# Optimization experiments

Measured on AMD Instinct MI355X. Metric: run time of the kernel, lower is better.

Reference implementation:

```python
import jax, jax.numpy as jnp
from jax import lax
import numpy as np

# Straight-through-estimator sign (standard BNN binarization):
# fwd: sign(x) with sign(0)=+1; bwd: pass gradient where |x|<=1 (hardtanh STE).
@jax.custom_vjp
def sign_ste(x):
    return jnp.where(x >= 0, 1.0, -1.0).astype(x.dtype)

def _sign_fwd(x):
    return sign_ste(x), x

def _sign_bwd(x, g):
    return (g * (jnp.abs(x) <= 1.0).astype(g.dtype),)

sign_ste.defvjp(_sign_fwd, _sign_bwd)

EPS = 1e-5  # BatchNorm eps (torch default)

def bn4(x, g, b):  # BatchNorm2d, training-mode batch stats, x: [N,C,H,W]
    m = x.mean((0, 2, 3), keepdims=True)
    v = x.var((0, 2, 3), keepdims=True)
    return g[None, :, None, None] * (x - m) * lax.rsqrt(v + EPS) + b[None, :, None, None]

def bn1(x, g, b):  # BatchNorm1d, x: [N,C]
    m = x.mean(0, keepdims=True)
    v = x.var(0, keepdims=True)
    return g * (x - m) * lax.rsqrt(v + EPS) + b

def bconv(x, W, b, first):
    # BinarizedConv2d: binarize weights always; binarize input except first layer.
    xb = x if first else sign_ste(x)
    y = lax.conv_general_dilated(xb, sign_ste(W), (1, 1), [(1, 1), (1, 1)],
                                 dimension_numbers=('NCHW', 'OIHW', 'NCHW'))
    return y + b[None, :, None, None]

def maxpool2(x):
    return lax.reduce_window(x, -jnp.inf, lax.max, (1, 1, 2, 2), (1, 1, 2, 2), 'VALID')

def ht(x):  # Hardtanh
    return jnp.clip(x, -1.0, 1.0)

CONV_CH = [(3, 64), (64, 128), (128, 256), (256, 256), (256, 512), (512, 512), (512, 512), (512, 512)]
LIN_CH = [(512, 512), (512, 512), (512, 10)]
POOL_AFTER = (0, 1, 3, 5, 7)  # conv indices followed by MaxPool2d

def setup_inputs():
    key = jax.random.key(0)
    ks = iter(jax.random.split(key, 64))
    d = {"x": jax.random.normal(next(ks), (256, 3, 32, 32), jnp.float32)}
    for i, (ci, co) in enumerate(CONV_CH):
        d[f"cw{i}"] = jax.random.normal(next(ks), (co, ci, 3, 3), jnp.float32) * 0.1
        d[f"cb{i}"] = jnp.zeros((co,), jnp.float32)
        d[f"cg{i}"] = jnp.ones((co,), jnp.float32)
        d[f"ct{i}"] = jnp.zeros((co,), jnp.float32)
    for i, (ci, co) in enumerate(LIN_CH):
        d[f"lw{i}"] = jax.random.normal(next(ks), (co, ci), jnp.float32) * 0.1
        d[f"lb{i}"] = jnp.zeros((co,), jnp.float32)
        d[f"lg{i}"] = jnp.ones((co,), jnp.float32)
        d[f"lt{i}"] = jnp.zeros((co,), jnp.float32)
    return d

def _forward(x, cw, cb, cg, ct, lw, lb, lg, lt):
    h = x
    for i in range(8):
        h = bconv(h, cw[i], cb[i], i == 0)
        if i in POOL_AFTER:
            h = maxpool2(h)
        h = ht(bn4(h, cg[i], ct[i]))
    h = h.reshape(h.shape[0], -1)  # [N, 512] after 5 pools on 32x32
    for i in range(3):
        h = sign_ste(h) @ sign_ste(lw[i]).T + lb[i]  # BinarizedLinear
        h = bn1(h, lg[i], lt[i])
        if i < 2:
            h = ht(h)  # Dropout is identity in eval mode
    return jax.nn.log_softmax(h, axis=-1)

def reference(x,
              cw0, cb0, cg0, ct0, cw1, cb1, cg1, ct1, cw2, cb2, cg2, ct2,
              cw3, cb3, cg3, ct3, cw4, cb4, cg4, ct4, cw5, cb5, cg5, ct5,
              cw6, cb6, cg6, ct6, cw7, cb7, cg7, ct7,
              lw0, lb0, lg0, lt0, lw1, lb1, lg1, lt1, lw2, lb2, lg2, lt2):
    cw = [cw0, cw1, cw2, cw3, cw4, cw5, cw6, cw7]
    cb = [cb0, cb1, cb2, cb3, cb4, cb5, cb6, cb7]
    cg = [cg0, cg1, cg2, cg3, cg4, cg5, cg6, cg7]
    ct = [ct0, ct1, ct2, ct3, ct4, ct5, ct6, ct7]
    lw = [lw0, lw1, lw2]
    lb = [lb0, lb1, lb2]
    lg = [lg0, lg1, lg2]
    lt = [lt0, lt1, lt2]
    return _forward(x, cw, cb, cg, ct, lw, lb, lg, lt)
```

## Files before the change

### kernel.cpp

```cpp
#include <hip/hip_runtime.h>
#include <hip/hip_bf16.h>

typedef unsigned long long u64;

#define EPSV 1e-5

__device__ __forceinline__ int imax(int a, int b) { return a > b ? a : b; }
__device__ __forceinline__ int iclamp(int v, int lo, int hi) { return v < lo ? lo : (v > hi ? hi : v); }

struct PrepArgs {
    const float* src[10];
    u64* dst[10];
    int CW[10];
    int Co[10];
    int taps[10];
    int rowbase[11];
    u64* accs;
    int naccs;
};

__global__ __launch_bounds__(256) void prep_kernel(PrepArgs a) {
    __shared__ float buf[4608];
    const int blk = blockIdx.x;
    int z = blk * 18 + threadIdx.x;
    if (threadIdx.x < 18 && z < a.naccs) a.accs[z] = 0ULL;

    int l = 0;
    while (l < 9 && blk >= a.rowbase[l + 1]) ++l;
    const int row = blk - a.rowbase[l];
    const int CW = a.CW[l];
    const int taps = a.taps[l];
    const int nf = CW * 64 * taps;
    const float* srow = a.src[l] + (size_t)row * nf;
    for (int i = threadIdx.x; i < nf; i += 256) buf[i] = srow[i];
    __syncthreads();
    const int t = threadIdx.x;
    if (t < taps * CW) {
        u64 bits = 0;
        if (taps == 9) {
            int k = t % 9, w = t / 9;
            for (int j = 0; j < 64; ++j) bits |= (u64)(buf[(w * 64 + j) * 9 + k] >= 0.f) << j;
            a.dst[l][(size_t)(k * CW + w) * a.Co[l] + row] = bits;
        } else {
            for (int j = 0; j < 64; ++j) bits |= (u64)(buf[t * 64 + j] >= 0.f) << j;
            a.dst[l][(size_t)row * CW + t] = bits;
        }
    }
}

__global__ __launch_bounds__(256) void conv0_lane(const float* __restrict__ x,
                                                  const float* __restrict__ wgt,
                                                  float* __restrict__ out,
                                                  double* __restrict__ dacc) {
    const int lane = threadIdx.x & 63;
    const int wave = threadIdx.x >> 6;
    float ws[27];
#pragma unroll
    for (int j = 0; j < 27; ++j) ws[j] = (wgt[lane * 27 + j] >= 0.f) ? 1.f : -1.f;

    const int gp0 = blockIdx.x * 32;
    const int n = gp0 >> 8;
    const int ypA = (gp0 >> 4) & 15;
    const int yb = 2 * ypA - 1;

    __shared__ float simg[3][6][34];
    const float* xb = x + (size_t)n * 3072;
    for (int t = threadIdx.x; t < 612; t += 256) {
        int ci = t / 204;
        int rem = t % 204;
        int r = rem / 34;
        int cc = rem % 34;
        int yy = yb + r;
        int xx = cc - 1;
        float v = 0.f;
        if ((unsigned)yy < 32u && (unsigned)xx < 32u) v = xb[(ci * 32 + yy) * 32 + xx];
        simg[ci][r][cc] = v;
    }
    __syncthreads();

    double s1 = 0.0, s2 = 0.0;
#pragma unroll 2
    for (int pi = 0; pi < 8; ++pi) {
        const int lp = wave * 8 + pi;
        const int gp = gp0 + lp;
        const int xp = lp & 15;
        const int rbase = 2 * (lp >> 4);
        const int cbase = 2 * xp;
        float win[3][4][4];
#pragma unroll
        for (int ci = 0; ci < 3; ++ci)
#pragma unroll
            for (int r = 0; r < 4; ++r)
#pragma unroll
                for (int c = 0; c < 4; ++c) win[ci][r][c] = simg[ci][rbase + r][cbase + c];
        float a00 = 0.f, a01 = 0.f, a10 = 0.f, a11 = 0.f;
#pragma unroll
        for (int ci = 0; ci < 3; ++ci)
#pragma unroll
            for (int ky = 0; ky < 3; ++ky)
#pragma unroll
                for (int kx = 0; kx < 3; ++kx) {
                    float wv = ws[ci * 9 + ky * 3 + kx];
                    a00 += win[ci][ky][kx] * wv;
                    a01 += win[ci][ky][kx + 1] * wv;
                    a10 += win[ci][ky + 1][kx] * wv;
                    a11 += win[ci][ky + 1][kx + 1] * wv;
                }
        float val = fmaxf(fmaxf(a00, a01), fmaxf(a10, a11));
        out[(size_t)gp * 64 + lane] = val;
        s1 += (double)val;
        s2 += (double)val * (double)val;
    }
    __shared__ double sh1[4][64], sh2[4][64];
    sh1[wave][lane] = s1;
    sh2[wave][lane] = s2;
    __syncthreads();
    if (threadIdx.x < 64) {
        double t1 = 0.0, t2 = 0.0;
#pragma unroll
        for (int r = 0; r < 4; ++r) { t1 += sh1[r][threadIdx.x]; t2 += sh2[r][threadIdx.x]; }
        double* sh = dacc + (size_t)(blockIdx.x & 7) * 1024;
        atomicAdd(&sh[2 * threadIdx.x], t1);
        atomicAdd(&sh[2 * threadIdx.x + 1], t2);
    }
}

__global__ __launch_bounds__(256) void bnpack_f(const float* __restrict__ in,
                                                const double* __restrict__ dacc,
                                                const float* __restrict__ g,
                                                const float* __restrict__ b,
                                                u64* __restrict__ act, int count) {
    __shared__ float2 sthr[64];
    if (threadIdx.x < 64) {
        int i = threadIdx.x;
        double S1 = 0.0, S2 = 0.0;
#pragma unroll
        for (int s = 0; s < 8; ++s) {
            S1 += dacc[s * 1024 + 2 * i];
            S2 += dacc[s * 1024 + 2 * i + 1];
        }
        double m = S1 / count;
        double var = S2 / count - m * m;
        double sc = (double)g[i] / sqrt(var + EPSV);
        float2 r;
        if (sc == 0.0) r = make_float2(b[i] >= 0.f ? -3.0e38f : 3.0e38f, 1.f);
        else {
            double t = m - (double)b[i] / sc;
            r = make_float2((float)t, sc > 0.0 ? 1.f : -1.f);
        }
        sthr[i] = r;
    }
    __syncthreads();
    int tid = blockIdx.x * 256 + threadIdx.x;
    int part = tid & 3;
    int word = tid >> 2;
    const float4* r4 = (const float4*)(in + (size_t)word * 64 + part * 16);
    u64 bits = 0;
#pragma unroll
    for (int q = 0; q < 4; ++q) {
        float4 v = r4[q];
        float vv[4] = {v.x, v.y, v.z, v.w};
#pragma unroll
        for (int u = 0; u < 4; ++u) {
            int c = part * 16 + q * 4 + u;
            float2 t = sthr[c];
            bool bit = (t.y > 0.f) ? (vv[u] >= t.x) : (vv[u] <= t.x);
            bits |= (u64)bit << c;
        }
    }
    bits |= __shfl_xor(bits, 1);
    bits |= __shfl_xor(bits, 2);
    if (part == 0) act[word] = bits;
}

__global__ __launch_bounds__(256) void bnpack_i(const short* __restrict__ in,
                                                const u64* __restrict__ iacc,
                                                const float* __restrict__ g,
                                                const float* __restrict__ b,
                                                u64* __restrict__ act, int Co, int wshift,
                                                int count) {
    __shared__ int2 sthr[520];
    for (int i = threadIdx.x; i < Co; i += 256) {
        long long S1 = 0, S2 = 0;
#pragma unroll
        for (int s = 0; s < 8; ++s) {
            S1 += (long long)iacc[s * 1024 + 2 * i];
            S2 += (long long)iacc[s * 1024 + 2 * i + 1];
        }
        double m = (double)S1 / count;
        double var = (double)S2 / count - m * m;
        double sc = (double)g[i] / sqrt(var + EPSV);
        int2 r;
        if (sc == 0.0) r = make_int2(b[i] >= 0.f ? (int)0x80000000 : 0x7fffffff, 0);
        else {
            double t = m - (double)b[i] / sc;
            if (t > 1.0e9) t = 1.0e9;
            if (t < -1.0e9) t = -1.0e9;
            r = (sc > 0.0) ? make_int2((int)ceil(t), 0) : make_int2((int)floor(t), 1);
        }
        sthr[(i >> 6) * 65 + (i & 63)] = r;
    }
    __syncthreads();
    int tid = blockIdx.x * 256 + threadIdx.x;
    int part = tid & 3;
    int word = tid >> 2;
    int w = word & ((1 << wshift) - 1);
    int pix = word >> wshift;
    const int4* r4 = (const int4*)(in + (size_t)pix * Co + (w << 6) + part * 16);
    u64 bits = 0;
#pragma unroll
    for (int q = 0; q < 2; ++q) {
        int4 v = r4[q];
        int words4[4] = {v.x, v.y, v.z, v.w};
#pragma unroll
        for (int u = 0; u < 4; ++u) {
#pragma unroll
            for (int h = 0; h < 2; ++h) {
                int c = part * 16 + q * 8 + u * 2 + h;
                int val = (int)(short)((h == 0) ? (words4[u] & 0xffff) : ((unsigned)words4[u] >> 16));
                int2 t = sthr[w * 65 + c];
                bool bit = t.y ? (val <= t.x) : (val >= t.x);
                bits |= (u64)bit << c;
            }
        }
    }
    bits |= __shfl_xor(bits, 1);
    bits |= __shfl_xor(bits, 2);
    if (part == 0) act[word] = bits;
}

template <int CW, int HIN, bool POOL, int WC, bool INTERIOR>
__device__ __forceinline__ void row_accum(const u64* __restrict__ inb,
                                          const u64* __restrict__ wpkT, int Co, int co,
                                          const int* yoff, const bool* ry, int* acc) {
    constexpr int HP = POOL ? HIN / 2 : HIN;
    constexpr int WS = POOL ? 4 : 3;
    constexpr int NA = POOL ? 4 : 1;
#pragma unroll 1
    for (int w0 = 0; w0 < CW; w0 += WC) {
        u64 wg[9 * WC];
#pragma unroll
        for (int k = 0; k < 9; ++k)
#pragma unroll
            for (int w = 0; w < WC; ++w)
                wg[k * WC + w] = wpkT[(size_t)(k * CW + w0 + w) * Co + co];
        u64 cur[WS][WS][WC];
#pragma unroll
        for (int d = 0; d < WS; ++d) {
            int cc = d - 1;
            int ccc = cc < 0 ? 0 : cc;
#pragma unroll
            for (int r = 0; r < WS; ++r) {
                const u64* p = inb + yoff[r] + ccc * CW + w0;
                if (WC == 1) {
                    cur[r][d][0] = p[0];
                } else {
                    ulonglong2 v = *(const ulonglong2*)p;
                    cur[r][d][0] = v.x;
                    cur[r][d][1] = v.y;
                }
            }
        }
#pragma unroll
        for (int xp = 0; xp < HP; ++xp) {
            if constexpr (POOL) {
#pragma unroll
                for (int py = 0; py < 2; ++py)
#pragma unroll
                    for (int qx = 0; qx < 2; ++qx)
#pragma unroll
                        for (int ky = 0; ky < 3; ++ky)
#pragma unroll
                            for (int kx = 0; kx < 3; ++kx) {
                                int d = qx + kx;
                                int cc = 2 * xp + d - 1;
                                if (cc >= 0 && cc < HIN) {
#pragma unroll
                                    for (int w = 0; w < WC; ++w) {
                                        int pcv = 64 - 2 * (int)__popcll(cur[py + ky][d][w] ^
                                                                         wg[(ky * 3 + kx) * WC + w]);
                                        if constexpr (INTERIOR)
                                            acc[xp * NA + py * 2 + qx] += pcv;
                                        else
                                            acc[xp * NA + py * 2 + qx] += ry[py + ky] ? pcv : 0;
                                    }
                                }
                            }
            } else {
#pragma unroll
                for (int ky = 0; ky < 3; ++ky)
#pragma unroll
                    for (int kx = 0; kx < 3; ++kx) {
                        int cc = xp + kx - 1;
                        if (cc >= 0 && cc < HIN) {
#pragma unroll
                            for (int w = 0; w < WC; ++w) {
                                int pcv = 64 - 2 * (int)__popcll(cur[ky][kx][w] ^
                                                                 wg[(ky * 3 + kx) * WC + w]);
                                if constexpr (INTERIOR)
                                    acc[xp] += pcv;
                                else
                                    acc[xp] += ry[ky] ? pcv : 0;
                            }
                        }
                    }
            }
            if (xp < HP - 1) {
                if constexpr (POOL) {
#pragma unroll
                    for (int r = 0; r < WS; ++r)
#pragma unroll
                        for (int w = 0; w < WC; ++w) {
                            cur[r][0][w] = cur[r][2][w];
                            cur[r][1][w] = cur[r][3][w];
                        }
#pragma unroll
                    for (int dd = 2; dd < 4; ++dd) {
                        int cc = 2 * (xp + 1) + dd - 1;
                        int ccc = cc >= HIN ? HIN - 1 : cc;
#pragma unroll
                        for (int r = 0; r < WS; ++r) {
                            const u64* p = inb + yoff[r] + ccc * CW + w0;
                            if (WC == 1) {
                                cur[r][dd][0] = p[0];
                            } else {
                                ulonglong2 v = *(const ulonglong2*)p;
                                cur[r][dd][0] = v.x;
                                cur[r][dd][1] = v.y;
                            }
                        }
                    }
                } else {
#pragma unroll
                    for (int r = 0; r < WS; ++r)
#pragma unroll
                        for (int w = 0; w < WC; ++w) {
                            cur[r][0][w] = cur[r][1][w];
                            cur[r][1][w] = cur[r][2][w];
                        }
                    int cc = xp + 2;
                    int ccc = cc >= HIN ? HIN - 1 : cc;
#pragma unroll
                    for (int r = 0; r < WS; ++r) {
                        const u64* p = inb + yoff[r] + ccc * CW + w0;
                        if (WC == 1) {
                            cur[r][2][0] = p[0];
                        } else {
                            ulonglong2 v = *(const ulonglong2*)p;
                            cur[r][2][0] = v.x;
                            cur[r][2][1] = v.y;
                        }
                    }
                }
            }
        }
    }
}

template <int CW, int HIN, bool POOL, int WC>
__global__ __launch_bounds__(256) void bconv_row(const u64* __restrict__ in,
                                                 const u64* __restrict__ wpkT,
                                                 short* __restrict__ out,
                                                 u64* __restrict__ iacc, int Co) {
    constexpr int HP = POOL ? HIN / 2 : HIN;
    constexpr int WS = POOL ? 4 : 3;
    constexpr int NA = POOL ? 4 : 1;
    const int lane = threadIdx.x & 63;
    const int co = blockIdx.y * 64 + lane;
    const int grow = blockIdx.x * 4 + (threadIdx.x >> 6);
    const int n = grow / HP;
    const int yp = grow % HP;
    const int y0 = (POOL ? 2 * yp : yp) - 1;
    const u64* inb = in + (size_t)n * (HIN * HIN * CW);
    int yoff[WS];
    bool ry[WS];
#pragma unroll
    for (int r = 0; r < WS; ++r) {
        int y = y0 + r;
        ry[r] = (unsigned)y < (unsigned)HIN;
        int yc = iclamp(y, 0, HIN - 1);
        yoff[r] = yc * HIN * CW;
    }
    int acc[HP * NA];
#pragma unroll
    for (int i = 0; i < HP * NA; ++i) acc[i] = 0;

    if (yp > 0 && yp < HP - 1)
        row_accum<CW, HIN, POOL, WC, true>(inb, wpkT, Co, co, yoff, ry, acc);
    else
        row_accum<CW, HIN, POOL, WC, false>(inb, wpkT, Co, co, yoff, ry, acc);

    int s1 = 0;
    long long s2 = 0;
    short* orow = out + (size_t)grow * HP * Co + co;
#pragma unroll
    for (int xp = 0; xp < HP; ++xp) {
        int ival;
        if constexpr (POOL)
            ival = imax(imax(acc[xp * 4], acc[xp * 4 + 1]), imax(acc[xp * 4 + 2], acc[xp * 4 + 3]));
        else
            ival = acc[xp];
        orow[(size_t)xp * Co] = (short)ival;
        s1 += ival;
        s2 += (long long)ival * ival;
    }

    __shared__ u64 sacc[128];
    if (threadIdx.x < 128) sacc[threadIdx.x] = 0ULL;
    __syncthreads();
    atomicAdd(&sacc[lane], (u64)(long long)s1);
    atomicAdd(&sacc[64 + lane], (u64)s2);
    __syncthreads();
    u64* sh = iacc + (size_t)(blockIdx.x & 7) * 1024;
    if (threadIdx.x < 64)
        atomicAdd(&sh[2 * (blockIdx.y * 64 + threadIdx.x)], sacc[threadIdx.x]);
    else if (threadIdx.x < 128)
        atomicAdd(&sh[2 * (blockIdx.y * 64 + threadIdx.x - 64) + 1], sacc[threadIdx.x]);
}

template <int CW, int HIN, bool POOL>
__global__ __launch_bounds__(256) void bconv_tiny(const u64* __restrict__ in,
                                                  const u64* __restrict__ wpkT,
                                                  short* __restrict__ out,
                                                  u64* __restrict__ iacc, int Co) {
    constexpr int NPX = HIN * HIN;
    constexpr int HP = POOL ? HIN / 2 : HIN;
    const int lane = threadIdx.x & 63;
    const int co = blockIdx.y * 64 + lane;
    const int n = blockIdx.x * 4 + (threadIdx.x >> 6);
    const u64* inb = in + (size_t)n * CW * NPX;
    int acc[NPX];
#pragma unroll
    for (int i = 0; i < NPX; ++i) acc[i] = 0;

#pragma unroll 2
    for (int w = 0; w < CW; ++w) {
        u64 win[NPX];
#pragma unroll
        for (int i = 0; i < NPX; ++i) win[i] = inb[i * CW + w];
#pragma unroll
        for (int k = 0; k < 9; ++k) {
            u64 wb = wpkT[(size_t)(k * CW + w) * Co + co];
            const int ky = k / 3, kx = k % 3;
#pragma unroll
            for (int py = 0; py < HIN; ++py)
#pragma unroll
                for (int px = 0; px < HIN; ++px) {
                    const int yy = py + ky - 1, xx = px + kx - 1;
                    if (yy >= 0 && yy < HIN && xx >= 0 && xx < HIN)
                        acc[py * HIN + px] += 64 - 2 * (int)__popcll(win[yy * HIN + xx] ^ wb);
                }
        }
    }

    short vals[HP * HP];
    if constexpr (POOL) {
#pragma unroll
        for (int py = 0; py < HP; ++py)
#pragma unroll
            for (int px = 0; px < HP; ++px)
                vals[py * HP + px] = (short)imax(
                    imax(acc[(2 * py) * HIN + 2 * px], acc[(2 * py) * HIN + 2 * px + 1]),
                    imax(acc[(2 * py + 1) * HIN + 2 * px], acc[(2 * py + 1) * HIN + 2 * px + 1]));
    } else {
#pragma unroll
        for (int i = 0; i < NPX; ++i) vals[i] = (short)acc[i];
    }
#pragma unroll
    for (int p = 0; p < HP * HP; ++p) out[(size_t)(n * HP * HP + p) * Co + co] = vals[p];

    long long s1 = 0, s2 = 0;
#pragma unroll
    for (int p = 0; p < HP * HP; ++p) {
        s1 += vals[p];
        s2 += (long long)vals[p] * vals[p];
    }
    __shared__ u64 sacc[128];
    if (threadIdx.x < 128) sacc[threadIdx.x] = 0ULL;
    __syncthreads();
    atomicAdd(&sacc[lane], (u64)s1);
    atomicAdd(&sacc[64 + lane], (u64)s2);
    __syncthreads();
    u64* sh = iacc + (size_t)(blockIdx.x & 7) * 1024;
    if (threadIdx.x < 64)
        atomicAdd(&sh[2 * (blockIdx.y * 64 + threadIdx.x)], sacc[threadIdx.x]);
    else if (threadIdx.x < 128)
        atomicAdd(&sh[2 * (blockIdx.y * 64 + threadIdx.x - 64) + 1], sacc[threadIdx.x]);
}

__global__ __launch_bounds__(256) void lin_kernel(const u64* __restrict__ hp,
                                                  const u64* __restrict__ wp,
                                                  const float* __restrict__ lb,
                                                  const float* __restrict__ g,
                                                  const float* __restrict__ bta,
                                                  float* __restrict__ z, int O, int applyHt) {
    int o = blockIdx.x;
    int n = threadIdx.x;
    const u64* hr = hp + n * 8;
    const u64* wr = wp + o * 8;
    int s = 0;
#pragma unroll
    for (int w = 0; w < 8; ++w) s += (int)__popcll(hr[w] ^ wr[w]);
    float val = (float)(512 - 2 * s) + lb[o];
    __shared__ double sh1[256], sh2[256];
    sh1[n] = (double)val;
    sh2[n] = (double)val * (double)val;
    __syncthreads();
    for (int st = 128; st > 0; st >>= 1) {
        if (n < st) {
            sh1[n] += sh1[n + st];
            sh2[n] += sh2[n + st];
        }
        __syncthreads();
    }
    __shared__ float sm, siv;
    if (n == 0) {
        double m = sh1[0] / 256.0;
        double var = sh2[0] / 256.0 - m * m;
        sm = (float)m;
        siv = (float)(1.0 / sqrt(var + EPSV));
    }
    __syncthreads();
    float zz = g[o] * (val - sm) * siv + bta[o];
    if (applyHt) zz = fminf(1.f, fmaxf(-1.f, zz));
    z[(size_t)n * O + o] = zz;
}

__global__ void pack_rows(const float* __restrict__ z, u64* __restrict__ hp) {
    int tid = blockIdx.x * 256 + threadIdx.x;
    int part = tid & 3;
    int word = tid >> 2;
    int ww = word & 7;
    int n = word >> 3;
    const float4* r4 = (const float4*)(z + (size_t)n * 512 + (ww << 6) + part * 16);
    u64 bits = 0;
#pragma unroll
    for (int q = 0; q < 4; ++q) {
        float4 v = r4[q];
        float vv[4] = {v.x, v.y, v.z, v.w};
#pragma unroll
        for (int u = 0; u < 4; ++u) bits |= (u64)(vv[u] >= 0.f) << (part * 16 + q * 4 + u);
    }
    bits |= __shfl_xor(bits, 1);
    bits |= __shfl_xor(bits, 2);
    if (part == 0) hp[word] = bits;
}

__global__ void lsm_kernel(const float* __restrict__ z, float* __restrict__ out) {
    int n = blockIdx.x * 64 + threadIdx.x;
    if (n >= 256) return;
    float v[10];
    float m = -1e30f;
#pragma unroll
    for (int i = 0; i < 10; ++i) {
        v[i] = z[n * 10 + i];
        m = fmaxf(m, v[i]);
    }
    float s = 0.f;
#pragma unroll
    for (int i = 0; i < 10; ++i) s += expf(v[i] - m);
    float ls = logf(s);
#pragma unroll
    for (int i = 0; i < 10; ++i) out[n * 10 + i] = v[i] - m - ls;
}

extern "C" void kernel_launch(void* const* d_in, const int* in_sizes, int n_in, void* d_out,
                              int out_size, void* d_ws, size_t ws_size, hipStream_t stream) {
    (void)in_sizes; (void)n_in; (void)out_size; (void)ws_size;
    const float* x = (const float*)d_in[0];
    const float *cw[8], *cb[8], *cg[8], *ct[8];
    for (int i = 0; i < 8; ++i) {
        cw[i] = (const float*)d_in[1 + 4 * i];
        cb[i] = (const float*)d_in[2 + 4 * i];
        cg[i] = (const float*)d_in[3 + 4 * i];
        ct[i] = (const float*)d_in[4 + 4 * i];
    }
    const float *lw[3], *lb[3], *lg[3], *lt[3];
    for (int i = 0; i < 3; ++i) {
        lw[i] = (const float*)d_in[33 + 4 * i];
        lb[i] = (const float*)d_in[34 + 4 * i];
        lg[i] = (const float*)d_in[35 + 4 * i];
        lt[i] = (const float*)d_in[36 + 4 * i];
    }

    static const int CIs[8] = {3, 64, 128, 256, 256, 512, 512, 512};
    static const int COs[8] = {64, 128, 256, 256, 512, 512, 512, 512};
    static const int HPs[8] = {16, 8, 8, 4, 4, 2, 2, 1};

    char* ws = (char*)d_ws;
    size_t off = 0;
    auto alloc = [&](size_t bytes) -> void* {
        void* p = ws + off;
        off += (bytes + 255) & ~(size_t)255;
        return p;
    };

    u64* wpkT[8] = {};
    for (int i = 1; i < 8; ++i) wpkT[i] = (u64*)alloc((size_t)COs[i] * 9 * (CIs[i] / 64) * 8);
    u64* wpl[3];
    int LO[3] = {512, 512, 10};
    for (int i = 0; i < 3; ++i) wpl[i] = (u64*)alloc((size_t)LO[i] * 8 * 8);
    u64* act[8];
    for (int i = 0; i < 8; ++i) act[i] = (u64*)alloc((size_t)256 * (COs[i] / 64) * HPs[i] * HPs[i] * 8);
    u64* fcs0 = (u64*)alloc(2048 * 8);
    u64* fcs1 = (u64*)alloc(2048 * 8);
    float* out0 = (float*)alloc((size_t)65536 * 64 * 4);
    short* i16A = (short*)alloc((size_t)16384 * 256 * 2);
    short* i16B = (short*)alloc((size_t)16384 * 256 * 2);
    float* z0 = (float*)alloc((size_t)256 * 512 * 4);
    float* z1 = (float*)alloc((size_t)256 * 512 * 4);
    float* z2 = (float*)alloc((size_t)256 * 10 * 4);
    u64* accs = (u64*)alloc((size_t)8 * 8 * 1024 * 8);
    double* dacc0 = (double*)accs;
    auto iacc = [&](int layer) { return accs + (size_t)layer * 8192; };

    PrepArgs pa;
    int rb = 0;
    for (int i = 1; i < 8; ++i) {
        int e = i - 1;
        pa.src[e] = cw[i];
        pa.dst[e] = wpkT[i];
        pa.CW[e] = CIs[i] / 64;
        pa.Co[e] = COs[i];
        pa.taps[e] = 9;
        pa.rowbase[e] = rb;
        rb += COs[i];
    }
    for (int i = 0; i < 3; ++i) {
        int e = 7 + i;
        pa.src[e] = lw[i];
        pa.dst[e] = wpl[i];
        pa.CW[e] = 8;
        pa.Co[e] = LO[i];
        pa.taps[e] = 1;
        pa.rowbase[e] = rb;
        rb += LO[i];
    }
    pa.rowbase[10] = rb;
    pa.accs = accs;
    pa.naccs = 8 * 8 * 1024;
    prep_kernel<<<rb, 256, 0, stream>>>(pa);

    conv0_lane<<<2048, 256, 0, stream>>>(x, cw[0], out0, dacc0);
    bnpack_f<<<1024, 256, 0, stream>>>(out0, dacc0, cg[0], ct[0], act[0], 65536);

    bconv_row<1, 16, true, 1><<<dim3(512, 2), 256, 0, stream>>>(act[0], wpkT[1], i16A, iacc(1), 128);
    bnpack_i<<<512, 256, 0, stream>>>(i16A, iacc(1), cg[1], ct[1], act[1], 128, 1, 16384);

    bconv_row<2, 8, false, 2><<<dim3(512, 4), 256, 0, stream>>>(act[1], wpkT[2], i16B, iacc(2), 256);
    bnpack_i<<<1024, 256, 0, stream>>>(i16B, iacc(2), cg[2], ct[2], act[2], 256, 2, 16384);

    bconv_row<4, 8, true, 2><<<dim3(256, 4), 256, 0, stream>>>(act[2], wpkT[3], i16A, iacc(3), 256);
    bnpack_i<<<256, 256, 0, stream>>>(i16A, iacc(3), cg[3], ct[3], act[3], 256, 2, 4096);

    bconv_row<4, 4, false, 2><<<dim3(256, 8), 256, 0, stream>>>(act[3], wpkT[4], i16B, iacc(4), 512);
    bnpack_i<<<512, 256, 0, stream>>>(i16B, iacc(4), cg[4], ct[4], act[4], 512, 3, 4096);

    bconv_tiny<8, 4, true><<<dim3(64, 8), 256, 0, stream>>>(act[4], wpkT[5], i16A, iacc(5), 512);
    bnpack_i<<<128, 256, 0, stream>>>(i16A, iacc(5), cg[5], ct[5], act[5], 512, 3, 1024);

    bconv_tiny<8, 2, false><<<dim3(64, 8), 256, 0, stream>>>(act[5], wpkT[6], i16B, iacc(6), 512);
    bnpack_i<<<128, 256, 0, stream>>>(i16B, iacc(6), cg[6], ct[6], act[6], 512, 3, 1024);

    bconv_tiny<8, 2, true><<<dim3(64, 8), 256, 0, stream>>>(act[6], wpkT[7], i16A, iacc(7), 512);
    bnpack_i<<<32, 256, 0, stream>>>(i16A, iacc(7), cg[7], ct[7], act[7], 512, 3, 256);

    lin_kernel<<<512, 256, 0, stream>>>(act[7], wpl[0], lb[0], lg[0], lt[0], z0, 512, 1);
    pack_rows<<<32, 256, 0, stream>>>(z0, fcs0);
    lin_kernel<<<512, 256, 0, stream>>>(fcs0, wpl[1], lb[1], lg[1], lt[1], z1, 512, 1);
    pack_rows<<<32, 256, 0, stream>>>(z1, fcs1);
    lin_kernel<<<10, 256, 0, stream>>>(fcs1, wpl[2], lb[2], lg[2], lt[2], z2, 10, 0);
    lsm_kernel<<<4, 64, 0, stream>>>(z2, (float*)d_out);
}
```

Baseline: 385.8 us.

## Vectorize loads in prep, conv0 and tiny conv; use shuffle reduction in linear

Several unrelated micro-optimizations are applied. The prep kernel copies weights with float4 loads, conv0 reads its shared-memory window with float2 loads, and bconv_tiny processes two packed input words per iteration using 128-bit loads. The linear kernel replaces its shared-memory tree reduction with wavefront shuffles plus a small cross-wave sum. These cut instruction and sync overhead in small kernels; the bconv_tiny change assumes CW is even and 16-byte alignment, and raises register pressure.

```diff
diff --git a/kernel.cpp b/kernel.cpp
--- a/kernel.cpp
+++ b/kernel.cpp
@@ -31,8 +31,9 @@
     const int CW = a.CW[l];
     const int taps = a.taps[l];
     const int nf = CW * 64 * taps;
-    const float* srow = a.src[l] + (size_t)row * nf;
-    for (int i = threadIdx.x; i < nf; i += 256) buf[i] = srow[i];
+    const float4* srow4 = (const float4*)(a.src[l] + (size_t)row * nf);
+    float4* buf4 = (float4*)buf;
+    for (int i = threadIdx.x; i < (nf >> 2); i += 256) buf4[i] = srow4[i];
     __syncthreads();
     const int t = threadIdx.x;
     if (t < taps * CW) {
@@ -82,7 +83,7 @@
 #pragma unroll 2
     for (int pi = 0; pi < 8; ++pi) {
         const int lp = wave * 8 + pi;
-        const int gp = gp0 + lp;
+        const int gp = gp0 + pi + wave * 8;
         const int xp = lp & 15;
         const int rbase = 2 * (lp >> 4);
         const int cbase = 2 * xp;
@@ -90,9 +91,14 @@
 #pragma unroll
         for (int ci = 0; ci < 3; ++ci)
 #pragma unroll
-            for (int r = 0; r < 4; ++r)
-#pragma unroll
-                for (int c = 0; c < 4; ++c) win[ci][r][c] = simg[ci][rbase + r][cbase + c];
+            for (int r = 0; r < 4; ++r) {
+                float2 t0 = *(const float2*)&simg[ci][rbase + r][cbase];
+                float2 t1 = *(const float2*)&simg[ci][rbase + r][cbase + 2];
+                win[ci][r][0] = t0.x;
+                win[ci][r][1] = t0.y;
+                win[ci][r][2] = t1.x;
+                win[ci][r][3] = t1.y;
+            }
         float a00 = 0.f, a01 = 0.f, a10 = 0.f, a11 = 0.f;
 #pragma unroll
         for (int ci = 0; ci < 3; ++ci)
@@ -433,22 +439,29 @@
 #pragma unroll
     for (int i = 0; i < NPX; ++i) acc[i] = 0;
 
-#pragma unroll 2
-    for (int w = 0; w < CW; ++w) {
-        u64 win[NPX];
-#pragma unroll
-        for (int i = 0; i < NPX; ++i) win[i] = inb[i * CW + w];
+#pragma unroll 1
+    for (int w = 0; w < CW; w += 2) {
+        u64 win[NPX][2];
+#pragma unroll
+        for (int i = 0; i < NPX; ++i) {
+            ulonglong2 v = *(const ulonglong2*)&inb[i * CW + w];
+            win[i][0] = v.x;
+            win[i][1] = v.y;
+        }
 #pragma unroll
         for (int k = 0; k < 9; ++k) {
-            u64 wb = wpkT[(size_t)(k * CW + w) * Co + co];
+            u64 wb0 = wpkT[(size_t)(k * CW + w) * Co + co];
+            u64 wb1 = wpkT[(size_t)(k * CW + w + 1) * Co + co];
             const int ky = k / 3, kx = k % 3;
 #pragma unroll
             for (int py = 0; py < HIN; ++py)
 #pragma unroll
                 for (int px = 0; px < HIN; ++px) {
                     const int yy = py + ky - 1, xx = px + kx - 1;
-                    if (yy >= 0 && yy < HIN && xx >= 0 && xx < HIN)
-                        acc[py * HIN + px] += 64 - 2 * (int)__popcll(win[yy * HIN + xx] ^ wb);
+                    if (yy >= 0 && yy < HIN && xx >= 0 && xx < HIN) {
+                        acc[py * HIN + px] += 64 - 2 * (int)__popcll(win[yy * HIN + xx][0] ^ wb0);
+                        acc[py * HIN + px] += 64 - 2 * (int)__popcll(win[yy * HIN + xx][1] ^ wb1);
+                    }
                 }
         }
     }
@@ -496,27 +509,28 @@
                                                   float* __restrict__ z, int O, int applyHt) {
     int o = blockIdx.x;
     int n = threadIdx.x;
+    const int lane = n & 63, wave = n >> 6;
     const u64* hr = hp + n * 8;
     const u64* wr = wp + o * 8;
     int s = 0;
 #pragma unroll
     for (int w = 0; w < 8; ++w) s += (int)__popcll(hr[w] ^ wr[w]);
     float val = (float)(512 - 2 * s) + lb[o];
-    __shared__ double sh1[256], sh2[256];
-    sh1[n] = (double)val;
-    sh2[n] = (double)val * (double)val;
-    __syncthreads();
-    for (int st = 128; st > 0; st >>= 1) {
-        if (n < st) {
-            sh1[n] += sh1[n + st];
-            sh2[n] += sh2[n + st];
-        }
-        __syncthreads();
-    }
+    double p1 = (double)val, p2 = (double)val * (double)val;
+#pragma unroll
+    for (int off = 32; off > 0; off >>= 1) {
+        p1 += __shfl_down(p1, off);
+        p2 += __shfl_down(p2, off);
+    }
+    __shared__ double w1[4], w2[4];
+    if (lane == 0) { w1[wave] = p1; w2[wave] = p2; }
+    __syncthreads();
     __shared__ float sm, siv;
     if (n == 0) {
-        double m = sh1[0] / 256.0;
-        double var = sh2[0] / 256.0 - m * m;
+        double S1 = w1[0] + w1[1] + w1[2] + w1[3];
+        double S2 = w2[0] + w2[1] + w2[2] + w2[3];
+        double m = S1 / 256.0;
+        double var = S2 / 256.0 - m * m;
         sm = (float)m;
         siv = (float)(1.0 / sqrt(var + EPSV));
     }
```

Result: slower. 401.1 us (+4.0%).
